# Kernel tuning notes

Hardware: AMD Instinct MI355X
Metric: run time of the kernel (lower is better)

## Reference

```python
import jax, jax.numpy as jnp
import numpy as np
from jax import lax

C = 512      # channels
K = 5        # dynamic_k
NH = 8       # num_heads
HID = 32     # channels // reduction
B, Hsp, Wsp = 8, 32, 32
EPS = 1e-5


def conv2d(x, w, b, pad):
    # x [B,Cin,H,W], w [Cout,Cin,kh,kw] -> NCHW conv (cross-correlation, like torch)
    y = lax.conv_general_dilated(x, w, (1, 1), [(pad, pad), (pad, pad)],
                                 dimension_numbers=('NCHW', 'OIHW', 'NCHW'))
    return y + b[None, :, None, None]


def setup_inputs() -> dict:
    key = jax.random.key(0)
    ks = jax.random.split(key, 20)
    s = 0.02
    inp = {
        'vi_feat': jax.random.normal(ks[0], (B, C, Hsp, Wsp), jnp.float32),
        'ir_feat': jax.random.normal(ks[1], (B, C, Hsp, Wsp), jnp.float32),
        # dynamic_conv: 1x1 convs treated as dense on pooled vector
        'dc_w1': jax.random.normal(ks[2], (4 * C, C), jnp.float32) * s,
        'dc_b1': jnp.zeros((4 * C,), jnp.float32),
        'dc_w2': jax.random.normal(ks[3], (K * K, 4 * C), jnp.float32) * s,
        'dc_b2': jnp.zeros((K * K,), jnp.float32),
        # cross-attention projections (torch MultiheadAttention layout: y = x @ W.T + b)
        'Wq': jax.random.normal(ks[4], (C, C), jnp.float32) * s,
        'bq': jnp.zeros((C,), jnp.float32),
        'Wk': jax.random.normal(ks[5], (C, C), jnp.float32) * s,
        'bk': jnp.zeros((C,), jnp.float32),
        'Wv': jax.random.normal(ks[6], (C, C), jnp.float32) * s,
        'bv': jnp.zeros((C,), jnp.float32),
        'Wo': jax.random.normal(ks[7], (C, C), jnp.float32) * s,
        'bo': jnp.zeros((C,), jnp.float32),
        # gate convs
        'gate_w1': jax.random.normal(ks[8], (HID, 2 * C, 3, 3), jnp.float32) * s,
        'gate_b1': jnp.zeros((HID,), jnp.float32),
        'gate_w2': jax.random.normal(ks[9], (2, HID, 3, 3), jnp.float32) * s,
        'gate_b2': jnp.zeros((2,), jnp.float32),
        # enhance: conv3x3 + BN (inference stats) + SiLU
        'enh_w': jax.random.normal(ks[10], (C, C, 3, 3), jnp.float32) * s,
        'enh_b': jnp.zeros((C,), jnp.float32),
        'bn_gamma': jnp.ones((C,), jnp.float32),
        'bn_beta': jnp.zeros((C,), jnp.float32),
        'bn_mean': jnp.zeros((C,), jnp.float32),
        'bn_var': jnp.ones((C,), jnp.float32),
    }
    return inp


def defa_forward(vi_feat, ir_feat, dc_w1, dc_b1, dc_w2, dc_b2,
                 Wq, bq, Wk, bk, Wv, bv, Wo, bo,
                 gate_w1, gate_b1, gate_w2, gate_b2,
                 enh_w, enh_b, bn_gamma, bn_beta, bn_mean, bn_var):
    b, c, h, w = vi_feat.shape
    n = h * w
    hd = c // NH

    # ---- dynamic_conv: GAP -> 1x1 -> ReLU -> 1x1 -> softmax over k^2 ----
    pooled = (vi_feat + ir_feat).mean(axis=(2, 3))                 # [B,C]
    hid = jax.nn.relu(pooled @ dc_w1.T + dc_b1)                    # [B,4C]
    kw = jax.nn.softmax(hid @ dc_w2.T + dc_b2, axis=1)             # [B,K*K]

    # ---- cross attention: query=vi, key=value=ir ----
    vi_seq = vi_feat.reshape(b, c, n).transpose(0, 2, 1)           # [B,N,C]
    ir_seq = ir_feat.reshape(b, c, n).transpose(0, 2, 1)
    q = (vi_seq @ Wq.T + bq).reshape(b, n, NH, hd)
    k_ = (ir_seq @ Wk.T + bk).reshape(b, n, NH, hd)
    v = (ir_seq @ Wv.T + bv).reshape(b, n, NH, hd)
    scores = jnp.einsum('bqhd,bkhd->bhqk', q, k_) / jnp.sqrt(jnp.float32(hd))
    attn = jax.nn.softmax(scores, axis=-1)
    ctx = jnp.einsum('bhqk,bkhd->bqhd', attn, v).reshape(b, n, c)
    fused_seq = ctx @ Wo.T + bo                                    # [B,N,C]
    fused_feat = fused_seq.transpose(0, 2, 1).reshape(b, c, h, w)

    # ---- dynamic per-pixel conv: unfold -> weighted sum == per-sample depthwise
    # correlation with the (shared-across-channels) KxK kernel kw ----
    ker = jnp.broadcast_to(kw.reshape(b, 1, 1, K, K), (b, c, 1, K, K))

    def one_sample(f, kk):  # f [C,H,W], kk [C,1,K,K]
        y = lax.conv_general_dilated(f[None], kk, (1, 1),
                                     [(K // 2, K // 2)] * 2,
                                     dimension_numbers=('NCHW', 'OIHW', 'NCHW'),
                                     feature_group_count=c)
        return y[0]

    dynamic_feat = jax.vmap(one_sample)(fused_feat, ker)           # [B,C,H,W]

    # ---- gated fusion ----
    gates = jax.nn.sigmoid(conv2d(jax.nn.relu(conv2d(
        jnp.concatenate([vi_feat, ir_feat], axis=1), gate_w1, gate_b1, 1)),
        gate_w2, gate_b2, 1))                                      # [B,2,H,W]
    w_vi, w_ir = gates[:, 0:1], gates[:, 1:2]
    fused = (w_ir * dynamic_feat + vi_feat) + (w_vi * dynamic_feat + ir_feat)

    # ---- enhance: conv3x3 + BN(inference) + SiLU ----
    y = conv2d(fused, enh_w, enh_b, 1)
    y = (y - bn_mean[None, :, None, None]) * (bn_gamma / jnp.sqrt(bn_var + EPS))[None, :, None, None] + bn_beta[None, :, None, None]
    return y * jax.nn.sigmoid(y)


def reference(vi_feat, ir_feat, dc_w1, dc_b1, dc_w2, dc_b2,
              Wq, bq, Wk, bk, Wv, bv, Wo, bo,
              gate_w1, gate_b1, gate_w2, gate_b2,
              enh_w, enh_b, bn_gamma, bn_beta, bn_mean, bn_var):
    return defa_forward(vi_feat, ir_feat, dc_w1, dc_b1, dc_w2, dc_b2,
                        Wq, bq, Wk, bk, Wv, bv, Wo, bo,
                        gate_w1, gate_b1, gate_w2, gate_b2,
                        enh_w, enh_b, bn_gamma, bn_beta, bn_mean, bn_var)
```

## Files before the change

### kernel.cpp

```cpp
#include <hip/hip_runtime.h>

typedef __bf16 bf16;
typedef __attribute__((ext_vector_type(2))) __bf16 bf16x2;
typedef __attribute__((ext_vector_type(4))) __bf16 bf16x4;
typedef __attribute__((ext_vector_type(8))) __bf16 bf16x8;
typedef __attribute__((ext_vector_type(4))) float f32x4;

constexpr size_t OFF_CATSEQ = 0;
constexpr size_t OFF_WBF    = 16777216;
constexpr size_t OFF_ENHW   = 18874368;
constexpr size_t OFF_GW1R   = 23592960;
constexpr size_t OFF_CHS    = 24182784;
constexpr size_t OFF_ZP     = 24186880;
constexpr size_t OFF_POOL   = 24187136;
constexpr size_t OFF_HID    = 24203520;
constexpr size_t OFF_KW     = 24269056;
constexpr size_t OFF_Q      = 24270080;
constexpr size_t OFF_K      = 32658688;
constexpr size_t OFF_VT     = 41047296;
constexpr size_t OFF_CTX    = 49435904;
constexpr size_t OFF_FF     = 57824512;
constexpr size_t OFF_G1P    = 66213120;
constexpr size_t OFF_Y1     = 75650304;
constexpr size_t OFF_GSUM   = 76698880;
constexpr size_t OFF_F2     = 76731648;

struct KParams {
  const float *vi, *ir, *bq, *bk, *bv, *bo, *gb1;
  char* ws;
  float* out;
};

__device__ __forceinline__ void gload16(const void* g, void* l) {
  __builtin_amdgcn_global_load_lds(
      (const __attribute__((address_space(1))) unsigned int*)g,
      (__attribute__((address_space(3))) unsigned int*)l, 16, 0, 0);
}

template<int N> __device__ __forceinline__ void waitvm() {
  if constexpr (N==0) asm volatile("s_waitcnt vmcnt(0)" ::: "memory");
  else if constexpr (N==1) asm volatile("s_waitcnt vmcnt(1)" ::: "memory");
  else if constexpr (N==2) asm volatile("s_waitcnt vmcnt(2)" ::: "memory");
  else if constexpr (N==3) asm volatile("s_waitcnt vmcnt(3)" ::: "memory");
  else if constexpr (N==4) asm volatile("s_waitcnt vmcnt(4)" ::: "memory");
  else if constexpr (N==6) asm volatile("s_waitcnt vmcnt(6)" ::: "memory");
  else if constexpr (N==8) asm volatile("s_waitcnt vmcnt(8)" ::: "memory");
  else asm volatile("s_waitcnt vmcnt(12)" ::: "memory");
}

__global__ __launch_bounds__(256) void k_wprep(const float* Wq, const float* Wk, const float* Wv, const float* Wo,
                        const float* enh_w, const float* gw1,
                        const float* enh_b, const float* gamma, const float* beta,
                        const float* mean, const float* var,
                        bf16* wbf, bf16* enhw, bf16* gw1r, float* chs, float* zp)
{
  __shared__ float ld[9216];
  int blk = blockIdx.x, tid = threadIdx.x;
  if (blk < 4099) {
    long i = (long)blk*256 + tid;
    if (i < 1048576) {
      int which = (int)(i >> 18); long r = i & 262143;
      const float* s = which==0?Wq: which==1?Wk: which==2?Wv:Wo;
      wbf[i] = (bf16)s[r];
    } else if (i < 1048576+512) {
      int c = (int)(i - 1048576);
      float sc = gamma[c]*rsqrtf(var[c]+1e-5f);
      chs[c] = sc; chs[512+c] = (enh_b[c]-mean[c])*sc + beta[c];
    } else if (i < 1048576+512+64) {
      zp[i - (1048576+512)] = 0.f;
    }
  } else if (blk < 4099+512) {
    int co = blk - 4099;
    const float* src = enh_w + (long)co*4608;
    #pragma unroll
    for (int it=0; it<18; ++it) ld[tid + 256*it] = src[tid + 256*it];
    __syncthreads();
    #pragma unroll
    for (int t=0;t<9;++t) {
      int ci = tid*2;
      bf16x2 v = { (bf16)ld[ci*9 + t], (bf16)ld[(ci+1)*9 + t] };
      ((bf16x2*)(enhw + (long)t*262144 + (long)co*512))[tid] = v;
    }
  } else {
    int hid = blk - (4099+512);
    const float* src = gw1 + (long)hid*9216;
    #pragma unroll
    for (int it=0; it<36; ++it) ld[tid + 256*it] = src[tid + 256*it];
    __syncthreads();
    #pragma unroll
    for (int t=0;t<9;++t) {
      int ci = tid*4;
      bf16x4 v = { (bf16)ld[ci*9+t], (bf16)ld[(ci+1)*9+t],
                   (bf16)ld[(ci+2)*9+t], (bf16)ld[(ci+3)*9+t] };
      *(bf16x4*)(gw1r + (long)t*32768 + (long)hid*1024 + ci) = v;
    }
  }
}

__global__ __launch_bounds__(256) void k_cat(const float* vi, const float* ir, bf16* cat, float* pool)
{
  __shared__ float ld[32][129];
  int pt = blockIdx.x, ct = blockIdx.y, b = blockIdx.z;
  const float* src = (ct < 16) ? vi : ir;
  int c0 = (ct & 15) * 32;
  int tid = threadIdx.x;
  int p0 = pt * 128;
  for (int it = 0; it < 4; ++it) {
    int row = it*8 + (tid>>5);
    int pc  = (tid & 31) * 4;
    float4 v = *(const float4*)(src + ((long)(b*512 + c0 + row))*1024 + p0 + pc);
    ld[row][pc+0]=v.x; ld[row][pc+1]=v.y; ld[row][pc+2]=v.z; ld[row][pc+3]=v.w;
  }
  __syncthreads();
  int p = tid >> 1, half = tid & 1;
  bf16x8 o0, o1;
  #pragma unroll
  for (int j = 0; j < 8; ++j) o0[j] = (bf16)ld[half*16 + j][p];
  #pragma unroll
  for (int j = 0; j < 8; ++j) o1[j] = (bf16)ld[half*16 + 8 + j][p];
  long ccol = (ct<16 ? 0 : 512) + c0 + half*16;
  bf16* dst = cat + ((long)(b*1024 + p0 + p))*1024 + ccol;
  *(bf16x8*)dst       = o0;
  *((bf16x8*)dst + 1) = o1;
  {
    int c = tid>>3, j = tid&7;
    float s = 0.f;
    #pragma unroll
    for (int i=0;i<16;++i) s += ld[c][j*16+i];
    s += __shfl_down(s, 4);
    s += __shfl_down(s, 2);
    s += __shfl_down(s, 1);
    if (j==0) {
      int pc_ = (ct<16 ? 0 : 512) + c0 + c;
      pool[((long)(b*8+pt))*1024 + pc_] = s;
    }
  }
}

__global__ __launch_bounds__(256) void k_mlp1(const float* partial, const float* w1, const float* b1, float* hid)
{
  __shared__ float pl[8*512];
  int tid = threadIdx.x;
  const float4* pp4 = (const float4*)partial;
  #pragma unroll
  for (int k=0;k<4;++k) {
    int j = tid + 256*k;
    int b = j>>7, c4 = j&127;
    float4 s = {0,0,0,0};
    #pragma unroll
    for (int pt=0;pt<8;++pt) {
      float4 v = pp4[(b*8+pt)*256 + c4];
      float4 w = pp4[(b*8+pt)*256 + 128 + c4];
      s.x+=v.x+w.x; s.y+=v.y+w.y; s.z+=v.z+w.z; s.w+=v.w+w.w;
    }
    float4 o = {s.x*(1.f/1024.f), s.y*(1.f/1024.f), s.z*(1.f/1024.f), s.w*(1.f/1024.f)};
    ((float4*)pl)[j] = o;
  }
  __syncthreads();
  int lane = tid&63, wave = tid>>6;
  #pragma unroll
  for (int rr=0; rr<4; ++rr) {
    int row = (blockIdx.x*4 + wave)*4 + rr;
    const float* wr = w1 + (long)row*512;
    float acc[8] = {};
    #pragma unroll
    for (int e=0;e<8;++e) {
      int c = lane + 64*e;
      float w = wr[c];
      #pragma unroll
      for (int b=0;b<8;++b) acc[b] += w * pl[b*512+c];
    }
    #pragma unroll
    for (int b=0;b<8;++b) {
      float s = acc[b];
      #pragma unroll
      for (int off=32; off; off>>=1) s += __shfl_down(s, off);
      if (lane==0) hid[b*2048 + row] = fmaxf(s + b1[row], 0.f);
    }
  }
}

__global__ __launch_bounds__(256) void k_mlp2a(const float* hid, const float* w2, const float* b2, float* lg)
{
  int blk = blockIdx.x; int b = blk/25, j = blk%25;
  int tid = threadIdx.x, lane = tid&63, wave = tid>>6;
  const float4* h4 = (const float4*)(hid + b*2048);
  const float4* w4 = (const float4*)(w2 + (long)j*2048);
  float4 a0 = h4[tid*2], a1 = h4[tid*2+1];
  float4 c0 = w4[tid*2], c1 = w4[tid*2+1];
  float s = a0.x*c0.x+a0.y*c0.y+a0.z*c0.z+a0.w*c0.w
          + a1.x*c1.x+a1.y*c1.y+a1.z*c1.z+a1.w*c1.w;
  #pragma unroll
  for (int off=32; off; off>>=1) s += __shfl_down(s, off);
  __shared__ float wsum[4];
  if (lane==0) wsum[wave] = s;
  __syncthreads();
  if (tid==0) lg[b*25+j] = wsum[0]+wsum[1]+wsum[2]+wsum[3] + b2[j];
}

__global__ __launch_bounds__(64) void k_smax(const float* lg, float* kw)
{
  int b = threadIdx.x;
  if (b < 8) {
    float mx = -1e30f;
    for (int j=0;j<25;++j) mx = fmaxf(mx, lg[b*25+j]);
    float e[25], s = 0.f;
    for (int j=0;j<25;++j){ e[j]=__expf(lg[b*25+j]-mx); s+=e[j]; }
    float inv = 1.f/s;
    for (int j=0;j<25;++j) kw[b*32+j] = e[j]*inv;
  }
}

template<int OP, int BM, int BN, int WAVES_M, int KSTEPS, int KU>
__global__ __launch_bounds__(256)
void k_gemm(KParams p)
{
  constexpr int WAVES_N = 4/WAVES_M;
  constexpr int MT = BM/(WAVES_M*16);
  constexpr int NT = BN/(WAVES_N*16);
  constexpr int ACH = (BM*4 + 255)/256;
  constexpr int BCH = (BN*4 + 255)/256;
  constexpr int WPS = KU*((BM*4)/256 + BCH);
  constexpr int NBUF = (KU==2) ? 2 : 3;
  __shared__ bf16 As[NBUF][KU*BM*32];
  __shared__ bf16 Bs[NBUF][KU*BN*32];
  const int tid = threadIdx.x, lane = tid&63, wave = tid>>6;
  const int g = lane>>4, l15 = lane&15;
  const int wm = wave % WAVES_M, wn = wave / WAVES_M;

  int b, which = 0, tapc = 0, kg = 0, m0, n0;
  const bf16 *Aptr, *Bptr;
  long ldb, lda;
  const int wg = blockIdx.x;
  if constexpr (OP==0) {
    b = wg&7; which = wg>>8;
    int xy = (wg>>3)&31;
    m0 = (xy>>3)*BM; n0 = (xy&7)*BN;
    Aptr = (const bf16*)(p.ws+OFF_WBF) + (long)which*262144;
    Bptr = (const bf16*)(p.ws+OFF_CATSEQ) + (long)b*1048576 + (which?512:0);
    ldb = 1024; lda = 512;
  } else if constexpr (OP==1) {
    b = wg&7;
    int xy = wg>>3;
    m0 = (xy>>3)*BM; n0 = (xy&7)*BN;
    Aptr = (const bf16*)(p.ws+OFF_WBF) + 3L*262144;
    Bptr = (const bf16*)(p.ws+OFF_CTX) + (long)b*524288;
    ldb = 512; lda = 512;
  } else if constexpr (OP==2) {
    b = wg&7;
    int loc = wg>>3;
    kg = loc>>5;
    int xy = loc&31;
    m0 = (xy>>3)*BM; n0 = (xy&7)*BN;
    Aptr = (const bf16*)(p.ws+OFF_ENHW);
    Bptr = (const bf16*)(p.ws+OFF_F2) + (long)b*524288;
    ldb = 512; lda = 512;
  } else {
    b = wg&7;
    int loc = wg>>3;
    tapc = loc>>3;
    m0 = 0; n0 = (loc&7)*BN;
    Aptr = (const bf16*)(p.ws+OFF_GW1R) + (long)tapc*32768;
    Bptr = (const bf16*)(p.ws+OFF_CATSEQ) + (long)b*1048576;
    ldb = 1024; lda = 1024;
  }
  const bf16* zp = (const bf16*)(p.ws+OFF_ZP);

  int tap = (OP==2) ? (kg*72)>>4 : tapc;
  int kcc = (OP==2) ? (kg*72)&15 : 0;
  const bf16* pA[ACH];
  const bf16* pB[BCH];
  bool aact[ACH];
  bool bval[BCH];
  int bpp[BCH], bss8[BCH];
  int dstA[ACH], dstB[BCH];
  #pragma unroll
  for (int i=0;i<ACH;++i) {
    int cc_ = tid + 256*i;
    aact[i] = cc_ < BM*4;
    int c = aact[i] ? cc_ : 0;
    int row = c>>2, slot = c&3, ss = slot ^ ((row>>1)&3);
    dstA[i] = ((c-lane))*8;
    if constexpr (OP==2) pA[i] = Aptr + (long)tap*262144 + (long)(m0+row)*lda + kcc*32 + ss*8;
    else                 pA[i] = Aptr + (long)(m0+row)*lda + ss*8;
  }
  #pragma unroll
  for (int i=0;i<BCH;++i) {
    int c = tid + 256*i;
    int row = c>>2, slot = c&3, ss = slot ^ ((row>>1)&3);
    dstB[i] = ((c-lane))*8;
    bss8[i] = ss*8;
    if constexpr (OP==2 || OP==3) {
      int pp = n0 + row; bpp[i] = pp;
      int hh = (pp>>5) + tap/3 - 1, ww = (pp&31) + tap%3 - 1;
      bool v = ((unsigned)hh < 32u) && ((unsigned)ww < 32u);
      bval[i] = v;
      pB[i] = v ? (Bptr + (long)(hh*32+ww)*ldb + kcc*32 + ss*8) : zp;
    } else {
      bval[i] = true;
      pB[i] = Bptr + (long)(n0+row)*ldb + ss*8;
    }
  }

  auto ADV = [&]() {
    if constexpr (OP==2) {
      ++kcc;
      if (kcc == 16) {
        kcc = 0; ++tap;
        int t3 = tap/3, tm = tap%3;
        #pragma unroll
        for (int i=0;i<ACH;++i) pA[i] += 262144 - 480;
        #pragma unroll
        for (int i=0;i<BCH;++i) {
          int hh = (bpp[i]>>5) + t3 - 1, ww = (bpp[i]&31) + tm - 1;
          bool v = ((unsigned)hh < 32u) && ((unsigned)ww < 32u);
          bval[i] = v;
          pB[i] = v ? (Bptr + (long)(hh*32+ww)*ldb + bss8[i]) : zp;
        }
      } else {
        #pragma unroll
        for (int i=0;i<ACH;++i) pA[i] += 32;
        #pragma unroll
        for (int i=0;i<BCH;++i) pB[i] += bval[i] ? 32 : 0;
      }
    } else if constexpr (OP==3) {
      #pragma unroll
      for (int i=0;i<ACH;++i) pA[i] += 32;
      #pragma unroll
      for (int i=0;i<BCH;++i) pB[i] += bval[i] ? 32 : 0;
    } else {
      #pragma unroll
      for (int i=0;i<ACH;++i) pA[i] += 32;
      #pragma unroll
      for (int i=0;i<BCH;++i) pB[i] += 32;
    }
  };

  auto STAGE = [&](int buf) {
    #pragma unroll
    for (int u=0;u<KU;++u) {
      #pragma unroll
      for (int i=0;i<ACH;++i) if (aact[i]) gload16(pA[i], As[buf] + u*BM*32 + dstA[i]);
      #pragma unroll
      for (int i=0;i<BCH;++i) gload16(pB[i], Bs[buf] + u*BN*32 + dstB[i]);
      ADV();
    }
  };

  f32x4 acc[MT][NT] = {};

  auto COMPUTE = [&](int cur) {
    #pragma unroll
    for (int u=0;u<KU;++u) {
      bf16x8 af[MT], bq_[NT];
      #pragma unroll
      for (int mt=0; mt<MT; ++mt) {
        int row = wm*MT*16 + mt*16 + l15;
        af[mt] = *(const bf16x8*)&As[cur][u*BM*32 + row*32 + 8*(g ^ ((row>>1)&3))];
      }
      #pragma unroll
      for (int nt=0; nt<NT; ++nt) {
        int row = wn*NT*16 + nt*16 + l15;
        bq_[nt] = *(const bf16x8*)&Bs[cur][u*BN*32 + row*32 + 8*(g ^ ((row>>1)&3))];
      }
      __builtin_amdgcn_s_setprio(1);
      #pragma unroll
      for (int mt=0; mt<MT; ++mt)
        #pragma unroll
        for (int nt=0; nt<NT; ++nt)
          acc[mt][nt] = __builtin_amdgcn_mfma_f32_16x16x32_bf16(af[mt], bq_[nt], acc[mt][nt], 0,0,0);
      __builtin_amdgcn_s_setprio(0);
    }
  };

  if constexpr (KU==2) {
    STAGE(0);
    int cur = 0;
    for (int ks = 0; ks < KSTEPS; ++ks) {
      if (ks+1 < KSTEPS) { STAGE(cur^1); waitvm<WPS>(); }
      else               { waitvm<0>(); }
      __builtin_amdgcn_s_barrier();
      __builtin_amdgcn_sched_barrier(0);
      COMPUTE(cur);
      __builtin_amdgcn_s_barrier();
      cur ^= 1;
    }
  } else {
    STAGE(0);
    STAGE(1);
    int cur = 0, stg = 2;
    for (int ks = 0; ks < KSTEPS; ++ks) {
      if (ks+2 < KSTEPS)      { STAGE(stg); stg = (stg==2)?0:stg+1; waitvm<2*WPS>(); }
      else if (ks+1 < KSTEPS) { waitvm<WPS>(); }
      else                    { waitvm<0>(); }
      __builtin_amdgcn_s_barrier();
      __builtin_amdgcn_sched_barrier(0);
      COMPUTE(cur);
      __builtin_amdgcn_s_barrier();
      cur = (cur==2)?0:cur+1;
    }
  }

  #pragma unroll
  for (int mt=0; mt<MT; ++mt) {
    #pragma unroll
    for (int nt=0; nt<NT; ++nt) {
      int mb = m0 + wm*MT*16 + mt*16 + 4*g;
      int n = n0 + wn*NT*16 + nt*16 + l15;
      if constexpr (OP==0) {
        const float* bias = which==0?p.bq: which==1?p.bk:p.bv;
        float v4[4];
        #pragma unroll
        for (int reg=0; reg<4; ++reg) {
          float v = acc[mt][nt][reg] + bias[mb+reg];
          if (which==0) v *= 0.18033688011112042f;
          v4[reg] = v;
        }
        int h = mb>>6, d0 = mb&63;
        if (which==2) {
          #pragma unroll
          for (int reg=0; reg<4; ++reg)
            ((bf16*)(p.ws+OFF_VT))[((long)(b*8+h)*64 + d0+reg)*1024 + n] = (bf16)v4[reg];
        } else {
          bf16* dst = (bf16*)(p.ws + (which==0?OFF_Q:OFF_K));
          bf16x4 o = {(bf16)v4[0],(bf16)v4[1],(bf16)v4[2],(bf16)v4[3]};
          *(bf16x4*)(dst + ((long)(b*8+h)*1024 + n)*64 + d0) = o;
        }
      } else {
        #pragma unroll
        for (int reg=0; reg<4; ++reg) {
          int m = mb + reg;
          float v = acc[mt][nt][reg];
          if constexpr (OP==1) {
            v += p.bo[m];
            ((bf16*)(p.ws+OFF_FF))[((long)(b*512+m))*1024 + n] = (bf16)v;
          } else if constexpr (OP==2) {
            float* part = (float*)(p.ws+OFF_Q) + (long)kg*4194304;
            part[((long)b*512+m)*1024 + n] = v;
          } else {
            ((float*)(p.ws+OFF_G1P))[((long)((tapc*8+b)*32+m))*1024 + n] = v;
          }
        }
      }
    }
  }
}

__global__ __launch_bounds__(256) void k_enhred(KParams p)
{
  long e = ((long)blockIdx.x*256 + threadIdx.x)*4;
  const float* part = (const float*)(p.ws+OFF_Q);
  float4 a = *(const float4*)(part + e);
  float4 c = *(const float4*)(part + 4194304 + e);
  int m = (int)((e>>10)&511);
  const float* chs = (const float*)(p.ws+OFF_CHS);
  float sc = chs[m], sh = chs[512+m];
  float4 o;
  float y0 = (a.x+c.x)*sc+sh, y1 = (a.y+c.y)*sc+sh, y2 = (a.z+c.z)*sc+sh, y3 = (a.w+c.w)*sc+sh;
  o.x = y0/(1.f+__expf(-y0)); o.y = y1/(1.f+__expf(-y1));
  o.z = y2/(1.f+__expf(-y2)); o.w = y3/(1.f+__expf(-y3));
  *(float4*)(p.out + e) = o;
}

__global__ __launch_bounds__(256)
void k_attn(KParams p)
{
  const bf16* Q = (const bf16*)(p.ws+OFF_Q);
  const bf16* K = (const bf16*)(p.ws+OFF_K);
  const bf16* V = (const bf16*)(p.ws+OFF_VT);
  bf16* ctx = (bf16*)(p.ws+OFF_CTX);
  int wg = blockIdx.x;
  int bh = (wg&7)*8 + (wg>>7);
  int qt = (wg>>3)&15;
  int b = bh>>3, h = bh&7;
  int tid = threadIdx.x, lane = tid&63, wave = tid>>6, g = lane>>4, l15 = lane&15;
  __shared__ bf16 Ks[2][64*64];
  __shared__ bf16 Vs[2][64*64];
  __shared__ bf16 Ps[4][16*64];
  const bf16* Qw = Q + ((long)bh*1024 + qt*64 + wave*16)*64;
  bf16x8 qf[2];
  qf[0] = *(const bf16x8*)(Qw + l15*64 + g*8);
  qf[1] = *(const bf16x8*)(Qw + l15*64 + 32 + g*8);
  const bf16* Kb = K + (long)bh*65536;
  const bf16* Vb = V + (long)bh*65536;
  float lrp[4] = {0,0,0,0};
  f32x4 cacc[4] = {};

  const bf16* pK[2]; const bf16* pV[2];
  int dstK[2], dstV[2];
  {
    int c = tid;
    int krow = c>>3, kslot = c&7, kss = kslot ^ (krow&7);
    pK[0] = Kb + (long)krow*64 + kss*8;
    pK[1] = Kb + (long)(krow+32)*64 + (kslot ^ ((krow+32)&7))*8;
    int d = c>>3, ss2 = kslot ^ (d&7);
    pV[0] = Vb + (long)d*1024 + ss2*8;
    pV[1] = Vb + (long)(d+32)*1024 + ss2*8;
    dstK[0] = (tid-lane)*8;       dstK[1] = (tid-lane+256)*8;
    dstV[0] = (tid-lane)*8;       dstV[1] = (tid-lane+256)*8;
  }
  auto STAGE = [&](int buf) {
    gload16(pK[0], Ks[buf] + dstK[0]);
    gload16(pK[1], Ks[buf] + dstK[1]);
    gload16(pV[0], Vs[buf] + dstV[0]);
    gload16(pV[1], Vs[buf] + dstV[1]);
  };
  auto ADV = [&]() {
    pK[0] += 4096; pK[1] += 4096;
    pV[0] += 64;   pV[1] += 64;
  };

  STAGE(0); ADV();
  int cur = 0;
  for (int step = 0; step < 16; ++step) {
    if (step < 15) { STAGE(cur^1); ADV(); waitvm<4>(); }
    else           { waitvm<0>(); }
    __builtin_amdgcn_s_barrier();
    __builtin_amdgcn_sched_barrier(0);
    f32x4 s0 = {}, s1 = {}, s2 = {}, s3 = {};
    __builtin_amdgcn_s_setprio(1);
    {
      int r0 = l15, r1 = 16+l15, r2 = 32+l15, r3 = 48+l15;
      #pragma unroll
      for (int ks2=0; ks2<2; ++ks2) {
        bf16x8 kf0 = *(const bf16x8*)&Ks[cur][r0*64 + 8*((4*ks2+g)^(r0&7))];
        bf16x8 kf1 = *(const bf16x8*)&Ks[cur][r1*64 + 8*((4*ks2+g)^(r1&7))];
        bf16x8 kf2 = *(const bf16x8*)&Ks[cur][r2*64 + 8*((4*ks2+g)^(r2&7))];
        bf16x8 kf3 = *(const bf16x8*)&Ks[cur][r3*64 + 8*((4*ks2+g)^(r3&7))];
        s0 = __builtin_amdgcn_mfma_f32_16x16x32_bf16(qf[ks2], kf0, s0, 0,0,0);
        s1 = __builtin_amdgcn_mfma_f32_16x16x32_bf16(qf[ks2], kf1, s1, 0,0,0);
        s2 = __builtin_amdgcn_mfma_f32_16x16x32_bf16(qf[ks2], kf2, s2, 0,0,0);
        s3 = __builtin_amdgcn_mfma_f32_16x16x32_bf16(qf[ks2], kf3, s3, 0,0,0);
      }
    }
    __builtin_amdgcn_s_setprio(0);
    bf16* Pw = Ps[wave];
    #pragma unroll
    for (int r=0;r<4;++r) {
      float p0 = __builtin_amdgcn_exp2f(s0[r]);
      float p1 = __builtin_amdgcn_exp2f(s1[r]);
      float p2 = __builtin_amdgcn_exp2f(s2[r]);
      float p3 = __builtin_amdgcn_exp2f(s3[r]);
      int q = 4*g + r;
      int xr = 8*(q&7);
      Pw[q*64 + ((     l15) ^ xr)] = (bf16)p0;
      Pw[q*64 + ((16 + l15) ^ xr)] = (bf16)p1;
      Pw[q*64 + ((32 + l15) ^ xr)] = (bf16)p2;
      Pw[q*64 + ((48 + l15) ^ xr)] = (bf16)p3;
      lrp[r] += (p0+p1)+(p2+p3);
    }
    bf16x8 pa0 = *(const bf16x8*)&Pw[l15*64 + 8*((  g)^(l15&7))];
    bf16x8 pa1 = *(const bf16x8*)&Pw[l15*64 + 8*((4+g)^(l15&7))];
    __builtin_amdgcn_s_setprio(1);
    #pragma unroll
    for (int nt=0;nt<4;++nt) {
      int d = nt*16 + l15;
      bf16x8 vf0 = *(const bf16x8*)&Vs[cur][d*64 + 8*((  g)^(d&7))];
      bf16x8 vf1 = *(const bf16x8*)&Vs[cur][d*64 + 8*((4+g)^(d&7))];
      cacc[nt] = __builtin_amdgcn_mfma_f32_16x16x32_bf16(pa0, vf0, cacc[nt], 0,0,0);
      cacc[nt] = __builtin_amdgcn_mfma_f32_16x16x32_bf16(pa1, vf1, cacc[nt], 0,0,0);
    }
    __builtin_amdgcn_s_setprio(0);
    __builtin_amdgcn_s_barrier();
    cur ^= 1;
  }
  float lr[4];
  #pragma unroll
  for (int r=0;r<4;++r) {
    float s = lrp[r];
    s += __shfl_xor(s, 1);
    s += __shfl_xor(s, 2);
    s += __shfl_xor(s, 4);
    s += __shfl_xor(s, 8);
    lr[r] = s;
  }
  #pragma unroll
  for (int nt=0;nt<4;++nt) {
    #pragma unroll
    for (int r=0;r<4;++r) {
      int q = qt*64 + wave*16 + 4*g + r;
      int cc = h*64 + nt*16 + l15;
      ctx[((long)(b*1024+q))*512 + cc] = (bf16)(cacc[nt][r] / lr[r]);
    }
  }
}

__global__ __launch_bounds__(256) void k_g1red(KParams p)
{
  long o = (long)blockIdx.x*256 + threadIdx.x;
  const float* part = (const float*)(p.ws+OFF_G1P);
  int m = (int)((o >> 10) & 31);
  float a = p.gb1[m];
  #pragma unroll
  for (int t=0;t<9;++t) a += part[(long)t*262144 + o];
  ((float*)(p.ws+OFF_Y1))[o] = fmaxf(a, 0.f);
}

__global__ __launch_bounds__(256)
void k_g2(KParams p, const float* gw2, const float* gb2)
{
  __shared__ float st[3*32*32];
  __shared__ float sg[2][32];
  int h = blockIdx.x, b = blockIdx.y;
  const float* y1 = (const float*)(p.ws+OFF_Y1) + (long)b*32768;
  int tid = threadIdx.x;
  for (int c = tid; c < 768; c += 256) {
    int e = c*4;
    int hr = e>>10, hid = (e>>5)&31, w = e&31;
    int hh = h + hr - 1;
    float4 v = {0,0,0,0};
    if ((unsigned)hh < 32u) v = *(const float4*)(y1 + hid*1024 + hh*32 + w);
    *(float4*)&st[e] = v;
  }
  __syncthreads();
  if (tid < 64) {
    int gg = tid>>5, w = tid&31;
    float acc = gb2[gg];
    for (int hid=0; hid<32; ++hid) {
      #pragma unroll
      for (int u=0;u<3;++u) {
        #pragma unroll
        for (int v=0;v<3;++v) {
          int ww = w + v - 1;
          if ((unsigned)ww < 32u)
            acc += st[(u*32+hid)*32 + ww] * gw2[((gg*32+hid)*3+u)*3+v];
        }
      }
    }
    sg[gg][w] = 1.f/(1.f+__expf(-acc));
  }
  __syncthreads();
  if (tid < 32) ((float*)(p.ws+OFF_GSUM))[b*1024 + h*32 + tid] = sg[0][tid]+sg[1][tid];
}

__global__ __launch_bounds__(512)
void k_dyn(KParams p)
{
  __shared__ float ffs[16*1024];
  int ct = blockIdx.x;
  int b  = blockIdx.y;
  int c0 = ct*16;
  int t = threadIdx.x;
  const bf16* ffg = (const bf16*)(p.ws+OFF_FF) + ((long)(b*512 + c0))*1024;
  #pragma unroll
  for (int k2 = 0; k2 < 4; ++k2) {
    int chunk = t + 512*k2;
    int c = chunk >> 7, j = chunk & 127;
    bf16x8 v = *(const bf16x8*)(ffg + (long)c*1024 + j*8);
    float* d = ffs + c*1024 + j*8;
    #pragma unroll
    for (int e=0;e<8;++e) d[e] = (float)v[e];
  }
  const float* kwp = (const float*)(p.ws+OFF_KW) + b*32;
  float kk[25];
  #pragma unroll
  for (int j=0;j<25;++j) kk[j] = kwp[j];
  __syncthreads();
  int w = t & 31;
  int h0 = t >> 5;
  #pragma unroll
  for (int pass=0; pass<2; ++pass) {
    int h = h0 + pass*16;
    int pos = h*32 + w;
    float gsw = ((const float*)(p.ws+OFF_GSUM))[b*1024 + pos];
    const bf16* cs = (const bf16*)(p.ws+OFF_CATSEQ) + ((long)(b*1024) + pos)*1024 + c0;
    bf16x8 vv0 = *(const bf16x8*)cs;
    bf16x8 vv1 = *(const bf16x8*)(cs + 8);
    bf16x8 rr0 = *(const bf16x8*)(cs + 512);
    bf16x8 rr1 = *(const bf16x8*)(cs + 520);
    bf16 outv[16];
    #pragma unroll
    for (int c=0;c<16;++c) {
      float dyn = 0.f;
      #pragma unroll
      for (int u=0;u<5;++u) {
        int hh = h+u-2;
        bool okh = (unsigned)hh < 32u;
        #pragma unroll
        for (int v=0;v<5;++v) {
          int ww = w+v-2;
          bool ok = okh && ((unsigned)ww < 32u);
          float fv = ffs[c*1024 + (hh&31)*32 + (ww&31)];
          dyn += (ok ? fv : 0.f) * kk[u*5+v];
        }
      }
      float resid = (c < 8) ? ((float)vv0[c] + (float)rr0[c])
                            : ((float)vv1[c-8] + (float)rr1[c-8]);
      float val = gsw*dyn + resid;
      outv[c] = (bf16)val;
    }
    bf16* f2 = (bf16*)(p.ws+OFF_F2) + ((long)(b*1024 + pos))*512 + c0;
    *(bf16x8*)f2       = *(bf16x8*)&outv[0];
    *((bf16x8*)f2 + 1) = *(bf16x8*)&outv[8];
  }
}

extern "C" void kernel_launch(void* const* d_in, const int* in_sizes, int n_in,
                              void* d_out, int out_size, void* d_ws, size_t ws_size,
                              hipStream_t stream)
{
  char* ws = (char*)d_ws;
  KParams p;
  p.vi = (const float*)d_in[0];  p.ir = (const float*)d_in[1];
  p.bq = (const float*)d_in[7];  p.bk = (const float*)d_in[9];
  p.bv = (const float*)d_in[11]; p.bo = (const float*)d_in[13];
  p.gb1 = (const float*)d_in[15];
  p.ws = ws; p.out = (float*)d_out;

  k_wprep<<<4643,256,0,stream>>>((const float*)d_in[6],(const float*)d_in[8],(const float*)d_in[10],(const float*)d_in[12],
      (const float*)d_in[18],(const float*)d_in[14],
      (const float*)d_in[19],(const float*)d_in[20],(const float*)d_in[21],(const float*)d_in[22],(const float*)d_in[23],
      (bf16*)(ws+OFF_WBF),(bf16*)(ws+OFF_ENHW),(bf16*)(ws+OFF_GW1R),(float*)(ws+OFF_CHS),(float*)(ws+OFF_ZP));
  k_cat<<<dim3(8,32,8),256,0,stream>>>(p.vi, p.ir, (bf16*)(ws+OFF_CATSEQ), (float*)(ws+OFF_Y1));
  k_mlp1<<<128,256,0,stream>>>((const float*)(ws+OFF_Y1),(const float*)d_in[2],(const float*)d_in[3],(float*)(ws+OFF_HID));
  k_mlp2a<<<200,256,0,stream>>>((const float*)(ws+OFF_HID),(const float*)d_in[4],(const float*)d_in[5],(float*)(ws+OFF_G1P));
  k_smax<<<1,64,0,stream>>>((const float*)(ws+OFF_G1P),(float*)(ws+OFF_KW));
  k_gemm<0,128,128,2,8,2><<<768,256,0,stream>>>(p);
  k_attn<<<1024,256,0,stream>>>(p);
  k_gemm<1,64,128,2,8,2><<<512,256,0,stream>>>(p);
  k_gemm<3,32,128,1,16,2><<<576,256,0,stream>>>(p);
  k_g1red<<<1024,256,0,stream>>>(p);
  k_g2<<<dim3(32,8),256,0,stream>>>(p,(const float*)d_in[16],(const float*)d_in[17]);
  k_dyn<<<dim3(32,8),512,0,stream>>>(p);
  k_gemm<2,128,128,2,36,2><<<512,256,0,stream>>>(p);
  k_enhred<<<4096,256,0,stream>>>(p);
}
```

Measured before the change: 222.7 us.

## Fuse cat into prep kernel and split-K reduction into enhance GEMM epilogue

Merges the input concatenation/transposition kernel into the weight-prep kernel, dropping one launch. It also removes the separate split-K reduction and BN+SiLU kernel: each enhance-GEMM tile atomically bumps a per-tile counter, and the second K-group block to finish adds the other partial and writes the activated output directly. This saves one full read pass over the partials plus a launch. In exchange it adds threadfence/atomic ordering, and the last-arriver still writes its own partial before combining.

```diff
diff --git a/kernel.cpp b/kernel.cpp
--- a/kernel.cpp
+++ b/kernel.cpp
@@ -48,15 +48,17 @@
   else asm volatile("s_waitcnt vmcnt(12)" ::: "memory");
 }
 
-__global__ __launch_bounds__(256) void k_wprep(const float* Wq, const float* Wk, const float* Wv, const float* Wo,
+__global__ __launch_bounds__(256) void k_prep(const float* vi, const float* ir,
+                        const float* Wq, const float* Wk, const float* Wv, const float* Wo,
                         const float* enh_w, const float* gw1,
                         const float* enh_b, const float* gamma, const float* beta,
                         const float* mean, const float* var,
-                        bf16* wbf, bf16* enhw, bf16* gw1r, float* chs, float* zp)
+                        bf16* wbf, bf16* enhw, bf16* gw1r, float* chs, float* zp,
+                        int* cnt, bf16* cat, float* pool)
 {
   __shared__ float ld[9216];
   int blk = blockIdx.x, tid = threadIdx.x;
-  if (blk < 4099) {
+  if (blk < 4100) {
     long i = (long)blk*256 + tid;
     if (i < 1048576) {
       int which = (int)(i >> 18); long r = i & 262143;
@@ -68,9 +70,11 @@
       chs[c] = sc; chs[512+c] = (enh_b[c]-mean[c])*sc + beta[c];
     } else if (i < 1048576+512+64) {
       zp[i - (1048576+512)] = 0.f;
-    }
-  } else if (blk < 4099+512) {
-    int co = blk - 4099;
+    } else if (i < 1048576+512+64+256) {
+      cnt[i - (1048576+512+64)] = 0;
+    }
+  } else if (blk < 4100+512) {
+    int co = blk - 4100;
     const float* src = enh_w + (long)co*4608;
     #pragma unroll
     for (int it=0; it<18; ++it) ld[tid + 256*it] = src[tid + 256*it];
@@ -81,8 +85,8 @@
       bf16x2 v = { (bf16)ld[ci*9 + t], (bf16)ld[(ci+1)*9 + t] };
       ((bf16x2*)(enhw + (long)t*262144 + (long)co*512))[tid] = v;
     }
-  } else {
-    int hid = blk - (4099+512);
+  } else if (blk < 4100+512+32) {
+    int hid = blk - (4100+512);
     const float* src = gw1 + (long)hid*9216;
     #pragma unroll
     for (int it=0; it<36; ++it) ld[tid + 256*it] = src[tid + 256*it];
@@ -94,45 +98,41 @@
                    (bf16)ld[(ci+2)*9+t], (bf16)ld[(ci+3)*9+t] };
       *(bf16x4*)(gw1r + (long)t*32768 + (long)hid*1024 + ci) = v;
     }
-  }
-}
-
-__global__ __launch_bounds__(256) void k_cat(const float* vi, const float* ir, bf16* cat, float* pool)
-{
-  __shared__ float ld[32][129];
-  int pt = blockIdx.x, ct = blockIdx.y, b = blockIdx.z;
-  const float* src = (ct < 16) ? vi : ir;
-  int c0 = (ct & 15) * 32;
-  int tid = threadIdx.x;
-  int p0 = pt * 128;
-  for (int it = 0; it < 4; ++it) {
-    int row = it*8 + (tid>>5);
-    int pc  = (tid & 31) * 4;
-    float4 v = *(const float4*)(src + ((long)(b*512 + c0 + row))*1024 + p0 + pc);
-    ld[row][pc+0]=v.x; ld[row][pc+1]=v.y; ld[row][pc+2]=v.z; ld[row][pc+3]=v.w;
-  }
-  __syncthreads();
-  int p = tid >> 1, half = tid & 1;
-  bf16x8 o0, o1;
-  #pragma unroll
-  for (int j = 0; j < 8; ++j) o0[j] = (bf16)ld[half*16 + j][p];
-  #pragma unroll
-  for (int j = 0; j < 8; ++j) o1[j] = (bf16)ld[half*16 + 8 + j][p];
-  long ccol = (ct<16 ? 0 : 512) + c0 + half*16;
-  bf16* dst = cat + ((long)(b*1024 + p0 + p))*1024 + ccol;
-  *(bf16x8*)dst       = o0;
-  *((bf16x8*)dst + 1) = o1;
-  {
-    int c = tid>>3, j = tid&7;
-    float s = 0.f;
-    #pragma unroll
-    for (int i=0;i<16;++i) s += ld[c][j*16+i];
-    s += __shfl_down(s, 4);
-    s += __shfl_down(s, 2);
-    s += __shfl_down(s, 1);
-    if (j==0) {
-      int pc_ = (ct<16 ? 0 : 512) + c0 + c;
-      pool[((long)(b*8+pt))*1024 + pc_] = s;
+  } else {
+    int idx = blk - (4100+512+32);
+    int pt = idx&7, ct = (idx>>3)&31, b = idx>>8;
+    const float* src = (ct < 16) ? vi : ir;
+    int c0 = (ct & 15) * 32;
+    int p0 = pt * 128;
+    for (int it = 0; it < 4; ++it) {
+      int row = it*8 + (tid>>5);
+      int pc  = (tid & 31) * 4;
+      float4 v = *(const float4*)(src + ((long)(b*512 + c0 + row))*1024 + p0 + pc);
+      ld[row*129+pc+0]=v.x; ld[row*129+pc+1]=v.y; ld[row*129+pc+2]=v.z; ld[row*129+pc+3]=v.w;
+    }
+    __syncthreads();
+    int p = tid >> 1, half = tid & 1;
+    bf16x8 o0, o1;
+    #pragma unroll
+    for (int j = 0; j < 8; ++j) o0[j] = (bf16)ld[(half*16 + j)*129 + p];
+    #pragma unroll
+    for (int j = 0; j < 8; ++j) o1[j] = (bf16)ld[(half*16 + 8 + j)*129 + p];
+    long ccol = (ct<16 ? 0 : 512) + c0 + half*16;
+    bf16* dst = cat + ((long)(b*1024 + p0 + p))*1024 + ccol;
+    *(bf16x8*)dst       = o0;
+    *((bf16x8*)dst + 1) = o1;
+    {
+      int c = tid>>3, j = tid&7;
+      float s = 0.f;
+      #pragma unroll
+      for (int i=0;i<16;++i) s += ld[c*129 + j*16+i];
+      s += __shfl_down(s, 4);
+      s += __shfl_down(s, 2);
+      s += __shfl_down(s, 1);
+      if (j==0) {
+        int pc_ = (ct<16 ? 0 : 512) + c0 + c;
+        pool[((long)(b*8+pt))*1024 + pc_] = s;
+      }
     }
   }
 }
@@ -228,7 +228,7 @@
   const int g = lane>>4, l15 = lane&15;
   const int wm = wave % WAVES_M, wn = wave / WAVES_M;
 
-  int b, which = 0, tapc = 0, kg = 0, m0, n0;
+  int b, which = 0, tapc = 0, kg = 0, m0, n0, xyv = 0;
   const bf16 *Aptr, *Bptr;
   long ldb, lda;
   const int wg = blockIdx.x;
@@ -251,6 +251,7 @@
     int loc = wg>>3;
     kg = loc>>5;
     int xy = loc&31;
+    xyv = xy;
     m0 = (xy>>3)*BM; n0 = (xy&7)*BN;
     Aptr = (const bf16*)(p.ws+OFF_ENHW);
     Bptr = (const bf16*)(p.ws+OFF_F2) + (long)b*524288;
@@ -444,22 +445,32 @@
       }
     }
   }
-}
-
-__global__ __launch_bounds__(256) void k_enhred(KParams p)
-{
-  long e = ((long)blockIdx.x*256 + threadIdx.x)*4;
-  const float* part = (const float*)(p.ws+OFF_Q);
-  float4 a = *(const float4*)(part + e);
-  float4 c = *(const float4*)(part + 4194304 + e);
-  int m = (int)((e>>10)&511);
-  const float* chs = (const float*)(p.ws+OFF_CHS);
-  float sc = chs[m], sh = chs[512+m];
-  float4 o;
-  float y0 = (a.x+c.x)*sc+sh, y1 = (a.y+c.y)*sc+sh, y2 = (a.z+c.z)*sc+sh, y3 = (a.w+c.w)*sc+sh;
-  o.x = y0/(1.f+__expf(-y0)); o.y = y1/(1.f+__expf(-y1));
-  o.z = y2/(1.f+__expf(-y2)); o.w = y3/(1.f+__expf(-y3));
-  *(float4*)(p.out + e) = o;
+
+  if constexpr (OP==2) {
+    __threadfence();
+    __shared__ int done_s;
+    if (tid==0) done_s = atomicAdd((int*)(p.ws+OFF_POOL) + (b*32 + xyv), 1);
+    __syncthreads();
+    if (done_s == 1) {
+      __threadfence();
+      const float* oth = (const float*)(p.ws+OFF_Q) + (long)(kg^1)*4194304;
+      const float* chs = (const float*)(p.ws+OFF_CHS);
+      #pragma unroll
+      for (int mt=0; mt<MT; ++mt) {
+        #pragma unroll
+        for (int nt=0; nt<NT; ++nt) {
+          #pragma unroll
+          for (int reg=0; reg<4; ++reg) {
+            int m = m0 + wm*MT*16 + mt*16 + 4*g + reg;
+            int n = n0 + wn*NT*16 + nt*16 + l15;
+            float v = acc[mt][nt][reg] + oth[((long)b*512+m)*1024 + n];
+            float y = v*chs[m] + chs[512+m];
+            p.out[((long)(b*512+m))*1024 + n] = y/(1.f+__expf(-y));
+          }
+        }
+      }
+    }
+  }
 }
 
 __global__ __launch_bounds__(256)
@@ -707,11 +718,12 @@
   p.gb1 = (const float*)d_in[15];
   p.ws = ws; p.out = (float*)d_out;
 
-  k_wprep<<<4643,256,0,stream>>>((const float*)d_in[6],(const float*)d_in[8],(const float*)d_in[10],(const float*)d_in[12],
+  k_prep<<<6692,256,0,stream>>>(p.vi, p.ir,
+      (const float*)d_in[6],(const float*)d_in[8],(const float*)d_in[10],(const float*)d_in[12],
       (const float*)d_in[18],(const float*)d_in[14],
       (const float*)d_in[19],(const float*)d_in[20],(const float*)d_in[21],(const float*)d_in[22],(const float*)d_in[23],
-      (bf16*)(ws+OFF_WBF),(bf16*)(ws+OFF_ENHW),(bf16*)(ws+OFF_GW1R),(float*)(ws+OFF_CHS),(float*)(ws+OFF_ZP));
-  k_cat<<<dim3(8,32,8),256,0,stream>>>(p.vi, p.ir, (bf16*)(ws+OFF_CATSEQ), (float*)(ws+OFF_Y1));
+      (bf16*)(ws+OFF_WBF),(bf16*)(ws+OFF_ENHW),(bf16*)(ws+OFF_GW1R),(float*)(ws+OFF_CHS),(float*)(ws+OFF_ZP),
+      (int*)(ws+OFF_POOL),(bf16*)(ws+OFF_CATSEQ),(float*)(ws+OFF_Y1));
   k_mlp1<<<128,256,0,stream>>>((const float*)(ws+OFF_Y1),(const float*)d_in[2],(const float*)d_in[3],(float*)(ws+OFF_HID));
   k_mlp2a<<<200,256,0,stream>>>((const float*)(ws+OFF_HID),(const float*)d_in[4],(const float*)d_in[5],(float*)(ws+OFF_G1P));
   k_smax<<<1,64,0,stream>>>((const float*)(ws+OFF_G1P),(float*)(ws+OFF_KW));
@@ -723,5 +735,4 @@
   k_g2<<<dim3(32,8),256,0,stream>>>(p,(const float*)d_in[16],(const float*)d_in[17]);
   k_dyn<<<dim3(32,8),512,0,stream>>>(p);
   k_gemm<2,128,128,2,36,2><<<512,256,0,stream>>>(p);
-  k_enhred<<<4096,256,0,stream>>>(p);
-}
+}
```

After: 323.1 us. +45.1%, slower.
